# Kernel optimization log

Hardware: AMD Instinct MI355X
Metric: run time of the kernel (lower is better)

## Reference

```python
import jax, jax.numpy as jnp
import numpy as np

# dims matching init_kwargs
D_MODEL = 2048
D_STATE = 64
D_CONV = 4
EXPAND = 2
HEADDIM = 128
NGROUPS = 1
CHUNK = 256
D_INNER = EXPAND * D_MODEL          # 4096
NHEADS = D_INNER // HEADDIM          # 32
CONV_DIM = D_INNER + 2 * NGROUPS * D_STATE      # 4224
D_IN_PROJ = 2 * D_INNER + 2 * NGROUPS * D_STATE + NHEADS  # 8352
BATCH = 2
SEQ = 4096  # multiple of CHUNK -> pad_to_block_length is a no-op
LN_EPS = 1e-5


def setup_inputs() -> dict:
    key = jax.random.key(0)
    ks = jax.random.split(key, 8)
    u = jax.random.normal(ks[0], (BATCH, SEQ, D_MODEL), jnp.float32)
    in_proj_w = jax.random.normal(ks[1], (D_IN_PROJ, D_MODEL), jnp.float32) * 0.02
    in_proj_b = jnp.zeros((D_IN_PROJ,), jnp.float32)
    conv_w = jax.random.normal(ks[2], (CONV_DIM, 1, D_CONV), jnp.float32) * 0.2
    conv_b = jnp.zeros((CONV_DIM,), jnp.float32)
    # dt_bias init as in the module (inverse-softplus of dt in [dt_min, dt_max])
    dt = jnp.exp(jax.random.uniform(ks[3], (NHEADS,), jnp.float32)
                 * (np.log(0.1) - np.log(0.001)) + np.log(0.001))
    dt_bias = dt + jnp.log(-jnp.expm1(-dt))
    A_log = jnp.log(jax.random.uniform(ks[4], (NHEADS,), jnp.float32, 1.0, 16.0))
    ln_w = jnp.ones((D_INNER,), jnp.float32)
    ln_b = jnp.zeros((D_INNER,), jnp.float32)
    out_proj_w = jax.random.normal(ks[5], (D_MODEL, D_INNER), jnp.float32) * 0.02
    out_proj_b = jnp.zeros((D_MODEL,), jnp.float32)
    return dict(u=u, in_proj_w=in_proj_w, in_proj_b=in_proj_b, conv_w=conv_w,
                conv_b=conv_b, dt_bias=dt_bias, A_log=A_log, ln_w=ln_w,
                ln_b=ln_b, out_proj_w=out_proj_w, out_proj_b=out_proj_b)


def segsum(x):
    """x: (..., T) -> (..., T, T) with segsum[i,j] = sum_{j<k<=i} x[k], -inf above diag."""
    T = x.shape[-1]
    lo = jnp.tril(jnp.ones((T, T), bool), -1)
    seg = jnp.cumsum(jnp.where(lo, x[..., :, None], 0.0), axis=-2)
    return jnp.where(jnp.tril(jnp.ones((T, T), bool), 0), seg, -jnp.inf)


def ssd_chunked(X, A, B, C):
    """X:(b,l,h,p) A:(b,l,h) B:(b,l,n) C:(b,l,n) (ngroups=1), chunked SSD scan."""
    b, l, h, p = X.shape
    c = l // CHUNK
    Xc = X.reshape(b, c, CHUNK, h, p)
    Ac = A.reshape(b, c, CHUNK, h).transpose(0, 3, 1, 2)  # b h c l
    Bc = B.reshape(b, c, CHUNK, -1)
    Cc = C.reshape(b, c, CHUNK, -1)
    A_cumsum = jnp.cumsum(Ac, axis=-1)                    # b h c l
    L = jnp.exp(segsum(Ac))                               # b h c l l
    Y_diag = jnp.einsum('bcln,bcsn,bhcls,bcshp->bclhp', Cc, Bc, L, Xc)
    decay_states = jnp.exp(A_cumsum[..., -1:] - A_cumsum)  # b h c l
    states = jnp.einsum('bcln,bhcl,bclhp->bchpn', Bc, decay_states, Xc)
    states = jnp.concatenate([jnp.zeros_like(states[:, :1]), states], axis=1)  # b (c+1) h p n
    A_last = jnp.pad(A_cumsum[..., -1], ((0, 0), (0, 0), (1, 0)))  # b h (c+1)
    decay_chunk = jnp.exp(segsum(A_last))                 # b h (c+1) (c+1)
    new_states = jnp.einsum('bhzc,bchpn->bzhpn', decay_chunk, states)
    inter_states = new_states[:, :-1]                     # b c h p n
    state_decay_out = jnp.exp(A_cumsum)                   # b h c l
    Y_off = jnp.einsum('bcln,bchpn,bhcl->bclhp', Cc, inter_states, state_decay_out)
    return (Y_diag + Y_off).reshape(b, l, h, p)


def reference(u, in_proj_w, in_proj_b, conv_w, conv_b, dt_bias, A_log,
              ln_w, ln_b, out_proj_w, out_proj_b):
    # seqlen already a multiple of CHUNK, so padding is a no-op
    zxbcdt = jnp.einsum('bld,ed->ble', u, in_proj_w) + in_proj_b
    A = -jnp.exp(A_log)                                   # (h,)
    z = zxbcdt[..., :D_INNER]
    xBC = zxbcdt[..., D_INNER:D_INNER + CONV_DIM]
    dt = jax.nn.softplus(zxbcdt[..., D_INNER + CONV_DIM:] + dt_bias)  # (b,l,h)
    # causal depthwise conv1d (pad left d_conv-1, crop to seqlen)
    x_ncl = jnp.transpose(xBC, (0, 2, 1))
    y_ncl = jax.lax.conv_general_dilated(
        x_ncl, conv_w, window_strides=(1,), padding=[(D_CONV - 1, 0)],
        feature_group_count=CONV_DIM, dimension_numbers=('NCH', 'OIH', 'NCH'))
    xBC = jax.nn.silu(jnp.transpose(y_ncl + conv_b[None, :, None], (0, 2, 1)))
    x = xBC[..., :D_INNER].reshape(*xBC.shape[:2], NHEADS, HEADDIM)  # b l h p
    Bm = xBC[..., D_INNER:D_INNER + NGROUPS * D_STATE]                # b l n
    Cm = xBC[..., D_INNER + NGROUPS * D_STATE:]                       # b l n
    y = ssd_chunked(x * dt[..., None], A * dt, Bm, Cm)
    y = y.reshape(*y.shape[:2], D_INNER)
    y = y * jax.nn.silu(z)
    mu = jnp.mean(y, axis=-1, keepdims=True)
    var = jnp.mean(jnp.square(y - mu), axis=-1, keepdims=True)
    y = (y - mu) * jax.lax.rsqrt(var + LN_EPS) * ln_w + ln_b
    out = jnp.einsum('bld,ed->ble', y, out_proj_w) + out_proj_b
    return out
```

## Files before the change

kernel.cpp:

```cpp
#include <hip/hip_runtime.h>
#include <math.h>

#define BATCH    2
#define SEQ      4096
#define DMODEL   2048
#define DSTATE   64
#define HEADDIM  128
#define NHEADS   32
#define DINNER   4096
#define CONVDIM  4224
#define DINPROJ  8352
#define NCHUNK   16
#define CHUNKL   256
#define ROWS     (BATCH*SEQ)

typedef __attribute__((ext_vector_type(8))) __bf16 bf16x8;
typedef __attribute__((ext_vector_type(4))) float floatx4;
typedef __attribute__((ext_vector_type(8))) unsigned short ushort8;
typedef __attribute__((ext_vector_type(2))) unsigned int uint2v;

__device__ __forceinline__ unsigned short f2bf(float f) {
    union { float f; unsigned int u; } v; v.f = f;
    unsigned int u = v.u;
    unsigned int r = (u + 0x7FFFu + ((u >> 16) & 1u)) >> 16;
    return (unsigned short)r;
}
__device__ __forceinline__ float bf2f(unsigned short s) {
    union { unsigned int u; float f; } v; v.u = ((unsigned int)s) << 16;
    return v.f;
}

__device__ __forceinline__ void gload_lds16(const unsigned short* g, unsigned short* lds) {
    __builtin_amdgcn_global_load_lds(
        (const __attribute__((address_space(1))) unsigned int*)g,
        (__attribute__((address_space(3))) unsigned int*)lds,
        16, 0, 0);
}

__device__ __forceinline__ uint2v tr16(const unsigned short* p) {
    uint2v d;
    asm volatile("ds_read_b64_tr_b16 %0, %1"
                 : "=v"(d)
                 : "v"((const __attribute__((address_space(3))) unsigned short*)p));
    return d;
}
union U8tr { uint2v v2[2]; bf16x8 f; };

__device__ __forceinline__ void cvt8(const float* s, unsigned short* d, int i) {
    float4 a = *reinterpret_cast<const float4*>(s + i);
    float4 b = *reinterpret_cast<const float4*>(s + i + 4);
    ushort8 o;
    o[0] = f2bf(a.x); o[1] = f2bf(a.y); o[2] = f2bf(a.z); o[3] = f2bf(a.w);
    o[4] = f2bf(b.x); o[5] = f2bf(b.y); o[6] = f2bf(b.z); o[7] = f2bf(b.w);
    *reinterpret_cast<ushort8*>(d + i) = o;
}

__global__ __launch_bounds__(256) void f32_to_bf16_2(
    const float* __restrict__ s0, unsigned short* __restrict__ d0, int nb0,
    const float* __restrict__ s1, unsigned short* __restrict__ d1)
{
    int b = blockIdx.x;
    if (b < nb0) {
        cvt8(s0, d0, (b * 256 + threadIdx.x) * 8);
    } else {
        cvt8(s1, d1, ((b - nb0) * 256 + threadIdx.x) * 8);
    }
}


#define STAGE(G, ldg, grow0, clampmax, k0, off)                                 \
  { int r0_ = (grow0) + sr0; int r1_ = (grow0) + sr1;                           \
    if ((clampmax) >= 0) { if (r0_ > (clampmax)) r0_ = (clampmax);              \
                           if (r1_ > (clampmax)) r1_ = (clampmax); }            \
    unsigned short* d_ = smem + (off) + ldsw;                                   \
    gload_lds16((G) + (size_t)r0_ * (ldg) + (k0) + sc0, d_);                    \
    gload_lds16((G) + (size_t)r1_ * (ldg) + (k0) + sc1, d_ + 4096); }

__device__ __forceinline__ void rd_a(bf16x8 (&dst)[4][2], const unsigned short* base) {
    #pragma unroll
    for (int mt = 0; mt < 4; ++mt)
        #pragma unroll
        for (int ks = 0; ks < 2; ++ks)
            dst[mt][ks] = *reinterpret_cast<const bf16x8*>(base + (mt * 2 + ks) * 512);
}
__device__ __forceinline__ void rd_b(bf16x8 (&dst)[2][2], const unsigned short* base) {
    #pragma unroll
    for (int nt = 0; nt < 2; ++nt)
        #pragma unroll
        for (int ks = 0; ks < 2; ++ks)
            dst[nt][ks] = *reinterpret_cast<const bf16x8*>(base + (nt * 2 + ks) * 512);
}

template<int R0, int C0>
__device__ __forceinline__ void mfma_q(floatx4 (&acc)[8][4],
                                       const bf16x8 (&a)[4][2],
                                       const bf16x8 (&b)[2][2])
{
    #pragma unroll
    for (int mt = 0; mt < 4; ++mt)
        #pragma unroll
        for (int nt = 0; nt < 2; ++nt) {
            acc[R0+mt][C0+nt] = __builtin_amdgcn_mfma_f32_16x16x32_bf16(a[mt][0], b[nt][0], acc[R0+mt][C0+nt], 0, 0, 0);
            acc[R0+mt][C0+nt] = __builtin_amdgcn_mfma_f32_16x16x32_bf16(a[mt][1], b[nt][1], acc[R0+mt][C0+nt], 0, 0, 0);
        }
}

#define MQ(R0, C0, A_, B_)                          \
    __builtin_amdgcn_s_setprio(1);                  \
    if (alive) mfma_q<R0, C0>(acc, A_, B_);         \
    __builtin_amdgcn_s_setprio(0);

template<int OUT_BF16>
__global__ __launch_bounds__(512, 2) void gemm256(
    const unsigned short* __restrict__ A, int lda,
    const unsigned short* __restrict__ Bt, int ldb,
    const float* __restrict__ bias,
    void* __restrict__ Cp, int ldc,
    int M, int N, int K)
{
    extern __shared__ __align__(16) unsigned short smem[];
    const int tid  = threadIdx.x;
    const int wave = tid >> 6;
    const int lane = tid & 63;
    const int q    = lane >> 4;
    const int lm   = lane & 15;
    const int wm   = wave >> 2;
    const int wn   = wave & 3;
    const int bh   = wn >> 1;
    const int bn2  = wn & 1;

    const int cpx = gridDim.x >> 3;
    const int sid = (blockIdx.x & 7) * cpx + (blockIdx.x >> 3);
    const int nbm = M >> 8;
    const int nbn = gridDim.x / nbm;
    int bm, bn;
    {
        const int GM = 8;
        int nig = GM * nbn;
        int grp = sid / nig;
        int first = grp * GM;
        int gsz = nbm - first; if (gsz > GM) gsz = GM;
        bm = first + (sid % nig) % gsz;
        bn = (sid % nig) / gsz;
    }
    const int arow0 = bm * 256;
    const int brow0 = bn * 256;
    const bool alive = (brow0 + wn * 64) < N;

    int sr0, sc0, sr1, sc1;
    {
        int L = tid << 4;
        int b = L & 1023; b ^= ((b >> 9) & 1) << 5;
        int sub = L >> 10;
        sr0 = ((sub >> 1) << 4) | (b >> 6);
        sc0 = ((sub & 1) << 5) | ((b & 63) >> 1);
        L = 8192 | (tid << 4);
        b = L & 1023; b ^= ((b >> 9) & 1) << 5;
        sub = L >> 10;
        sr1 = ((sub >> 1) << 4) | (b >> 6);
        sc1 = ((sub & 1) << 5) | ((b & 63) >> 1);
    }
    const int ldsw = wave * 512;
    const int lhw = ((((lm << 6) | (q << 4)) ^ ((lm & 8) << 2)) >> 1);
    const int NT  = K >> 6;
    const int NM1 = N - 1;

    STAGE(A,  lda, arow0,       -1,  0,  0);
    STAGE(A,  lda, arow0 + 128, -1,  0,  8192);
    STAGE(Bt, ldb, brow0,       NM1, 0,  16384);
    STAGE(Bt, ldb, brow0 + 128, NM1, 0,  24576);
    STAGE(Bt, ldb, brow0,       NM1, 64, 32768 + 16384);
    STAGE(Bt, ldb, brow0 + 128, NM1, 64, 32768 + 24576);
    STAGE(A,  lda, arow0,       -1,  64, 32768);
    STAGE(A,  lda, arow0 + 128, -1,  64, 32768 + 8192);
    asm volatile("s_waitcnt vmcnt(8)" ::: "memory");
    __builtin_amdgcn_s_barrier();

    const unsigned short* Ab0 = smem + wm * 8192 + lhw;
    const unsigned short* Bb0 = smem + 16384 + bh * 8192 + bn2 * 4096 + lhw;
    const unsigned short* Ab1 = Ab0 + 32768;
    const unsigned short* Bb1 = Bb0 + 32768;

    bf16x8 a_lo[4][2], a_hi[4][2], b_lo[2][2], b_hi[2][2];
    rd_a(a_lo, Ab0);
    rd_b(b_lo, Bb0);

    floatx4 acc[8][4] = {};
    const int NI = NT >> 1;

    for (int i = 0; i < NI; ++i) {
        int tE2 = 2 * i + 2; if (tE2 > NT - 1) tE2 = NT - 1;
        int tO2 = 2 * i + 3; if (tO2 > NT - 1) tO2 = NT - 1;
        const int kE = tE2 << 6, kO = tO2 << 6;

        rd_b(b_hi, Bb0 + 2048);
        __builtin_amdgcn_s_barrier();
        MQ(0, 0, a_lo, b_lo);
        __builtin_amdgcn_s_barrier();

        rd_a(a_hi, Ab0 + 4096);
        STAGE(Bt, ldb, brow0, NM1, kE, 16384);
        __builtin_amdgcn_s_barrier();
        MQ(0, 2, a_lo, b_hi);
        __builtin_amdgcn_s_barrier();

        STAGE(Bt, ldb, brow0 + 128, NM1, kE, 24576);
        STAGE(A,  lda, arow0,       -1,  kE, 0);
        __builtin_amdgcn_s_barrier();
        MQ(4, 2, a_hi, b_hi);
        asm volatile("s_waitcnt vmcnt(6)" ::: "memory");
        __builtin_amdgcn_s_barrier();

        rd_a(a_lo, Ab1);
        rd_b(b_hi, Bb1);
        STAGE(A, lda, arow0 + 128, -1, kE, 8192);
        __builtin_amdgcn_s_barrier();
        MQ(4, 0, a_hi, b_lo);
        __builtin_amdgcn_s_barrier();

        rd_b(b_lo, Bb1 + 2048);
        __builtin_amdgcn_s_barrier();
        MQ(0, 0, a_lo, b_hi);
        __builtin_amdgcn_s_barrier();

        rd_a(a_hi, Ab1 + 4096);
        STAGE(Bt, ldb, brow0, NM1, kO, 32768 + 16384);
        __builtin_amdgcn_s_barrier();
        MQ(0, 2, a_lo, b_lo);
        __builtin_amdgcn_s_barrier();

        STAGE(Bt, ldb, brow0 + 128, NM1, kO, 32768 + 24576);
        STAGE(A,  lda, arow0,       -1,  kO, 32768);
        __builtin_amdgcn_s_barrier();
        MQ(4, 2, a_hi, b_lo);
        asm volatile("s_waitcnt vmcnt(6)" ::: "memory");
        __builtin_amdgcn_s_barrier();

        rd_a(a_lo, Ab0);
        rd_b(b_lo, Bb0);
        STAGE(A, lda, arow0 + 128, -1, kO, 32768 + 8192);
        __builtin_amdgcn_s_barrier();
        MQ(4, 0, a_hi, b_hi);
        __builtin_amdgcn_s_barrier();
    }

    asm volatile("s_waitcnt vmcnt(0)" ::: "memory");

    const int row0 = arow0 + wm * 128;
    const int col0 = brow0 + wn * 64;
    #pragma unroll
    for (int mt = 0; mt < 8; ++mt)
        #pragma unroll
        for (int nt = 0; nt < 4; ++nt) {
            int col = col0 + nt * 16 + lm;
            if (col < N) {
                float bv = bias[col];
                #pragma unroll
                for (int r = 0; r < 4; ++r) {
                    int row = row0 + mt * 16 + q * 4 + r;
                    float v = acc[mt][nt][r] + bv;
                    if (OUT_BF16)
                        ((unsigned short*)Cp)[(size_t)row * ldc + col] = f2bf(v);
                    else
                        ((float*)Cp)[(size_t)row * ldc + col] = v;
                }
            }
        }
}

#define NCONVB (ROWS * (CONVDIM / 8) / 256)

__global__ __launch_bounds__(256) void convdt(
    const unsigned short* __restrict__ zx, const float* __restrict__ conv_w,
    const float* __restrict__ conv_b, unsigned short* __restrict__ xBC,
    const float* __restrict__ dt_bias, const float* __restrict__ A_log,
    float* __restrict__ dtb, float* __restrict__ cum, float* __restrict__ csum)
{
    __shared__ float ws4[4];
    if (blockIdx.x < NCONVB) {
        int idx = blockIdx.x * 256 + threadIdx.x;
        int g   = idx % (CONVDIM / 8);
        int row = idx / (CONVDIM / 8);
        int l   = row & (SEQ - 1);
        int ch0 = g * 8;
        const unsigned short* base = zx + (size_t)row * DINPROJ + DINNER + ch0;
        float s[8];
        float4 w4[8];
        #pragma unroll
        for (int c = 0; c < 8; ++c) {
            s[c]  = conv_b[ch0 + c];
            w4[c] = *reinterpret_cast<const float4*>(conv_w + (ch0 + c) * 4);
        }
        #pragma unroll
        for (int j = 0; j < 4; ++j) {
            int lj = l - 3 + j;
            if (lj >= 0) {
                ushort8 v = *reinterpret_cast<const ushort8*>(base + (long)(lj - l) * DINPROJ);
                #pragma unroll
                for (int c = 0; c < 8; ++c) {
                    float wj = (j == 0) ? w4[c].x : (j == 1) ? w4[c].y : (j == 2) ? w4[c].z : w4[c].w;
                    s[c] += wj * bf2f(v[c]);
                }
            }
        }
        ushort8 o;
        #pragma unroll
        for (int c = 0; c < 8; ++c) {
            float sig = 1.f / (1.f + __expf(-s[c]));
            o[c] = f2bf(s[c] * sig);
        }
        *reinterpret_cast<ushort8*>(xBC + (size_t)row * CONVDIM + ch0) = o;
    } else {
        int id = blockIdx.x - NCONVB;
        int h  = id & 31;
        int c  = (id >> 5) & 15;
        int b  = id >> 9;
        int t  = threadIdx.x;
        int row = b * SEQ + c * CHUNKL + t;
        float v = bf2f(zx[(size_t)row * DINPROJ + DINNER + CONVDIM + h]) + dt_bias[h];
        float dtv = (v > 20.f) ? v : log1pf(__expf(v));
        dtb[row * NHEADS + h] = dtv;
        float adt = -__expf(A_log[h]) * dtv;
        int lane = t & 63, wv = t >> 6;
        float s = adt;
        #pragma unroll
        for (int o = 1; o < 64; o <<= 1) {
            float x = __shfl_up(s, o, 64);
            if (lane >= o) s += x;
        }
        if (lane == 63) ws4[wv] = s;
        __syncthreads();
        float basev = 0.f;
        #pragma unroll
        for (int w = 0; w < 3; ++w)
            if (w < wv) basev += ws4[w];
        s += basev;
        cum[id * 256 + t] = s;
        if (t == 255) csum[id] = s;
    }
}

__global__ __launch_bounds__(256) void score_kernel(
    const unsigned short* __restrict__ xBC, unsigned short* __restrict__ S_raw)
{
    int bc = blockIdx.x;
    int sq = blockIdx.y;
    int tid = threadIdx.x;
    int wave = tid >> 6, lane = tid & 63, q = lane >> 4, lm = lane & 15;
    __shared__ __align__(16) unsigned short Ct[256 * 72];
    __shared__ __align__(16) unsigned short Btl[64 * 72];

    #pragma unroll
    for (int i = 0; i < 8; ++i) {
        int idx = tid + 256 * i;
        int r = idx >> 3, ch = idx & 7;
        ushort8 v = *reinterpret_cast<const ushort8*>(
            &xBC[(size_t)(bc * 256 + r) * CONVDIM + DINNER + DSTATE + ch * 8]);
        *reinterpret_cast<ushort8*>(&Ct[r * 72 + ch * 8]) = v;
    }
    #pragma unroll
    for (int i = 0; i < 2; ++i) {
        int idx = tid + 256 * i;
        int r = idx >> 3, ch = idx & 7;
        ushort8 v = *reinterpret_cast<const ushort8*>(
            &xBC[(size_t)(bc * 256 + sq * 64 + r) * CONVDIM + DINNER + ch * 8]);
        *reinterpret_cast<ushort8*>(&Btl[r * 72 + ch * 8]) = v;
    }
    __syncthreads();

    floatx4 acc[4][4] = {};
    #pragma unroll
    for (int ks = 0; ks < 2; ++ks) {
        bf16x8 af[4], bfv[4];
        #pragma unroll
        for (int mt = 0; mt < 4; ++mt)
            af[mt] = *reinterpret_cast<const bf16x8*>(&Ct[(wave * 64 + mt * 16 + lm) * 72 + ks * 32 + q * 8]);
        #pragma unroll
        for (int nt = 0; nt < 4; ++nt)
            bfv[nt] = *reinterpret_cast<const bf16x8*>(&Btl[(nt * 16 + lm) * 72 + ks * 32 + q * 8]);
        #pragma unroll
        for (int mt = 0; mt < 4; ++mt)
            #pragma unroll
            for (int nt = 0; nt < 4; ++nt)
                acc[mt][nt] = __builtin_amdgcn_mfma_f32_16x16x32_bf16(af[mt], bfv[nt], acc[mt][nt], 0, 0, 0);
    }

    #pragma unroll
    for (int mt = 0; mt < 4; ++mt)
        #pragma unroll
        for (int nt = 0; nt < 4; ++nt) {
            int l = wave * 64 + mt * 16 + q * 4;
            int s = sq * 64 + nt * 16 + lm;
            #pragma unroll
            for (int r = 0; r < 4; ++r)
                S_raw[(size_t)(bc * 256 + l + r) * 256 + s] = f2bf(acc[mt][nt][r]);
        }
}

__global__ __launch_bounds__(256) void states_kernel(
    const unsigned short* __restrict__ xBC, const float* __restrict__ dtb,
    const float* __restrict__ cum, float* __restrict__ states)
{
    int id = blockIdx.x;
    int h  = id & 31;
    int c  = (id >> 5) & 15;
    int b  = id >> 9;
    int tid = threadIdx.x;
    int wave = tid >> 6, lane = tid & 63, q = lane >> 4, lm = lane & 15;

    __shared__ float wls[256];
    __shared__ __align__(16) unsigned short Xs[16 * 8 * 72];
    __shared__ __align__(16) unsigned short Bs[16 * 4 * 72];

    const int cumbase = id * 256;
    const int row0 = b * SEQ + c * CHUNKL;
    {
        float cumlast = cum[cumbase + 255];
        wls[tid] = __expf(cumlast - cum[cumbase + tid]) * dtb[(row0 + tid) * NHEADS + h];
    }

    floatx4 acc[2][4] = {};

    for (int sc = 0; sc < 4; ++sc) {
        const int s0 = sc * 64;
        __syncthreads();
        #pragma unroll
        for (int i = 0; i < 4; ++i) {
            int idx = tid + 256 * i;
            int sr = idx >> 4, ch = idx & 15;
            int row = row0 + s0 + sr;
            ushort8 v = *reinterpret_cast<const ushort8*>(
                &xBC[(size_t)row * CONVDIM + h * HEADDIM + ch * 8]);
            float w = wls[s0 + sr];
            ushort8 o;
            #pragma unroll
            for (int j = 0; j < 8; ++j) o[j] = f2bf(bf2f(v[j]) * w);
            int a = ((sr >> 2) * 8 + (ch >> 1)) * 72 + (sr & 3) * 16 + (ch & 1) * 8;
            *reinterpret_cast<ushort8*>(&Xs[a]) = o;
        }
        #pragma unroll
        for (int i = 0; i < 2; ++i) {
            int idx = tid + 256 * i;
            int sr = idx >> 3, ch = idx & 7;
            int row = row0 + s0 + sr;
            ushort8 v = *reinterpret_cast<const ushort8*>(
                &xBC[(size_t)row * CONVDIM + DINNER + ch * 8]);
            int a = ((sr >> 2) * 4 + (ch >> 1)) * 72 + (sr & 3) * 16 + (ch & 1) * 8;
            *reinterpret_cast<ushort8*>(&Bs[a]) = v;
        }
        __syncthreads();
        #pragma unroll
        for (int ks = 0; ks < 2; ++ks) {
            bf16x8 af[2], bfv[4];
            #pragma unroll
            for (int mt = 0; mt < 2; ++mt) {
                const unsigned short* vp = Xs + ((ks * 8 + 2 * q) * 8 + (wave * 2 + mt)) * 72 + lm * 4;
                U8tr u; u.v2[0] = tr16(vp); u.v2[1] = tr16(vp + 576);
                af[mt] = u.f;
            }
            #pragma unroll
            for (int nt = 0; nt < 4; ++nt) {
                const unsigned short* vp = Bs + ((ks * 8 + 2 * q) * 4 + nt) * 72 + lm * 4;
                U8tr u; u.v2[0] = tr16(vp); u.v2[1] = tr16(vp + 288);
                bfv[nt] = u.f;
            }
            asm volatile("s_waitcnt lgkmcnt(0)" ::: "memory");
            __builtin_amdgcn_sched_barrier(0);
            #pragma unroll
            for (int mt = 0; mt < 2; ++mt)
                #pragma unroll
                for (int nt = 0; nt < 4; ++nt)
                    acc[mt][nt] = __builtin_amdgcn_mfma_f32_16x16x32_bf16(af[mt], bfv[nt], acc[mt][nt], 0, 0, 0);
        }
    }

    #pragma unroll
    for (int mt = 0; mt < 2; ++mt)
        #pragma unroll
        for (int nt = 0; nt < 4; ++nt)
            #pragma unroll
            for (int r = 0; r < 4; ++r) {
                int p = wave * 32 + mt * 16 + q * 4 + r;
                int n = nt * 16 + lm;
                states[(size_t)id * 8192 + p * 64 + n] = acc[mt][nt][r];
            }
}

__global__ __launch_bounds__(256) void inter_kernel(
    float* __restrict__ states, const float* __restrict__ csum)
{
    int idx = blockIdx.x * 256 + threadIdx.x;
    int pn  = idx & 8191;
    int h   = (idx >> 13) & 31;
    int b   = idx >> 18;
    float S = 0.f;
    for (int c = 0; c < 16; ++c) {
        int id = (b * 16 + c) * 32 + h;
        size_t off = (size_t)id * 8192 + pn;
        float st = states[off];
        states[off] = S;
        S = S * __expf(csum[id]) + st;
    }
}

__global__ __launch_bounds__(256) void y_mfma(
    const unsigned short* __restrict__ xBC,
    const unsigned short* __restrict__ S_raw,
    const float* __restrict__ dtb,
    const float* __restrict__ cum,
    const float* __restrict__ inter,
    unsigned short* __restrict__ zx)
{
    int id = blockIdx.x;
    int h  = id & 31;
    int bc = id >> 5;
    const int lh = blockIdx.y;
    int tid = threadIdx.x, wave = tid >> 6, lane = tid & 63, q = lane >> 4, lm = lane & 15;
    int wl = wave >> 1, wp = wave & 1;

    __shared__ float cums[256];
    __shared__ float dts[256];
    __shared__ __align__(16) unsigned short XdtT[128 * 72];
    __shared__ __align__(16) unsigned short PT[128 * 72];

    cums[tid] = cum[id * 256 + tid];
    dts[tid]  = dtb[(size_t)(bc * 256 + tid) * NHEADS + h];
    __syncthreads();

    floatx4 acc[4][4] = {};
    const int l0w = lh * 128 + wl * 64;
    const int nst = 2 * lh + 2;

    for (int st = 0; st < nst; ++st) {
        const int s0 = st * 64;
        __syncthreads();
        #pragma unroll
        for (int i = 0; i < 4; ++i) {
            int idx = tid + 256 * i;
            int sr = idx >> 4, ch = idx & 15;
            int srow = bc * 256 + s0 + sr;
            ushort8 v = *reinterpret_cast<const ushort8*>(
                &xBC[(size_t)srow * CONVDIM + h * HEADDIM + ch * 8]);
            float dt = dts[s0 + sr];
            ushort8 o;
            #pragma unroll
            for (int j = 0; j < 8; ++j) o[j] = f2bf(bf2f(v[j]) * dt);
            int a = ((sr >> 2) * 8 + (ch >> 1)) * 72 + (sr & 3) * 16 + (ch & 1) * 8;
            *reinterpret_cast<ushort8*>(&XdtT[a]) = o;
        }
        const int r0 = (s0 > lh * 128) ? 64 : 0;
        const int iters = (128 - r0) >> 5;
        for (int i = 0; i < iters; ++i) {
            int idx = tid + 256 * i;
            int r = r0 + (idx >> 3), ch = idx & 7;
            int l = lh * 128 + r;
            float cl = cums[l];
            ushort8 v = *reinterpret_cast<const ushort8*>(
                &S_raw[(size_t)(bc * 256 + l) * 256 + s0 + ch * 8]);
            ushort8 o;
            #pragma unroll
            for (int j = 0; j < 8; ++j) {
                int s = s0 + ch * 8 + j;
                float val = (s <= l) ? bf2f(v[j]) * __expf(cl - cums[s]) : 0.f;
                o[j] = f2bf(val);
            }
            *reinterpret_cast<ushort8*>(&PT[r * 72 + ch * 8]) = o;
        }
        __syncthreads();
        if (s0 <= l0w) {
            #pragma unroll
            for (int ks = 0; ks < 2; ++ks) {
                bf16x8 af[4], bfv[4];
                #pragma unroll
                for (int mt = 0; mt < 4; ++mt)
                    af[mt] = *reinterpret_cast<const bf16x8*>(
                        &PT[(wl * 64 + mt * 16 + lm) * 72 + ks * 32 + q * 8]);
                #pragma unroll
                for (int nt = 0; nt < 4; ++nt) {
                    const unsigned short* vp = XdtT + ((ks * 8 + 2 * q) * 8 + (wp * 4 + nt)) * 72 + lm * 4;
                    U8tr u; u.v2[0] = tr16(vp); u.v2[1] = tr16(vp + 576);
                    bfv[nt] = u.f;
                }
                asm volatile("s_waitcnt lgkmcnt(0)" ::: "memory");
                __builtin_amdgcn_sched_barrier(0);
                #pragma unroll
                for (int mt = 0; mt < 4; ++mt)
                    #pragma unroll
                    for (int nt = 0; nt < 4; ++nt)
                        acc[mt][nt] = __builtin_amdgcn_mfma_f32_16x16x32_bf16(af[mt], bfv[nt], acc[mt][nt], 0, 0, 0);
            }
        }
    }

    __syncthreads();
    {
        int p = tid >> 1, n0 = (tid & 1) * 32;
        const float* sp = &inter[(size_t)id * 8192 + p * 64 + n0];
        #pragma unroll
        for (int k2 = 0; k2 < 4; ++k2) {
            float4 a = *reinterpret_cast<const float4*>(sp + k2 * 8);
            float4 b2 = *reinterpret_cast<const float4*>(sp + k2 * 8 + 4);
            ushort8 o;
            o[0] = f2bf(a.x); o[1] = f2bf(a.y); o[2] = f2bf(a.z); o[3] = f2bf(a.w);
            o[4] = f2bf(b2.x); o[5] = f2bf(b2.y); o[6] = f2bf(b2.z); o[7] = f2bf(b2.w);
            *reinterpret_cast<ushort8*>(&XdtT[p * 72 + n0 + k2 * 8]) = o;
        }
        int r = tid >> 1;
        int l = lh * 128 + r;
        float ef = __expf(cums[l]);
        const unsigned short* cp = &xBC[(size_t)(bc * 256 + l) * CONVDIM + DINNER + DSTATE + n0];
        #pragma unroll
        for (int k2 = 0; k2 < 4; ++k2) {
            ushort8 v = *reinterpret_cast<const ushort8*>(cp + k2 * 8);
            ushort8 o;
            #pragma unroll
            for (int j = 0; j < 8; ++j) o[j] = f2bf(bf2f(v[j]) * ef);
            *reinterpret_cast<ushort8*>(&PT[r * 72 + n0 + k2 * 8]) = o;
        }
    }
    __syncthreads();
    #pragma unroll
    for (int ks = 0; ks < 2; ++ks) {
        bf16x8 af[4], bfv[4];
        #pragma unroll
        for (int mt = 0; mt < 4; ++mt)
            af[mt] = *reinterpret_cast<const bf16x8*>(
                &PT[(wl * 64 + mt * 16 + lm) * 72 + ks * 32 + q * 8]);
        #pragma unroll
        for (int nt = 0; nt < 4; ++nt)
            bfv[nt] = *reinterpret_cast<const bf16x8*>(
                &XdtT[(wp * 64 + nt * 16 + lm) * 72 + ks * 32 + q * 8]);
        #pragma unroll
        for (int mt = 0; mt < 4; ++mt)
            #pragma unroll
            for (int nt = 0; nt < 4; ++nt)
                acc[mt][nt] = __builtin_amdgcn_mfma_f32_16x16x32_bf16(af[mt], bfv[nt], acc[mt][nt], 0, 0, 0);
    }

    #pragma unroll
    for (int mt = 0; mt < 4; ++mt)
        #pragma unroll
        for (int nt = 0; nt < 4; ++nt) {
            int l = lh * 128 + wl * 64 + mt * 16 + q * 4;
            int pcol = wp * 64 + nt * 16 + lm;
            #pragma unroll
            for (int r = 0; r < 4; ++r)
                zx[(size_t)(bc * 256 + l + r) * DINPROJ + DINNER + h * HEADDIM + pcol]
                    = f2bf(acc[mt][nt][r]);
        }
}

__global__ __launch_bounds__(256) void gate_ln_cvt(
    unsigned short* __restrict__ zx, const float* __restrict__ ln_w,
    const float* __restrict__ ln_b,
    const float* __restrict__ w2, unsigned short* __restrict__ w2_bf)
{
    __shared__ float rs[256], rq[256];
    if (blockIdx.x >= ROWS) {
        cvt8(w2, w2_bf, ((blockIdx.x - ROWS) * 256 + threadIdx.x) * 8);
        return;
    }
    int row = blockIdx.x;
    int t   = threadIdx.x;
    size_t base = (size_t)row * DINPROJ;
    float g[16];
    float sum = 0.f, sumsq = 0.f;
    #pragma unroll
    for (int j = 0; j < 2; ++j) {
        int i = t * 8 + j * 2048;
        ushort8 zv = *reinterpret_cast<const ushort8*>(zx + base + i);
        ushort8 yv = *reinterpret_cast<const ushort8*>(zx + base + DINNER + i);
        #pragma unroll
        for (int k = 0; k < 8; ++k) {
            float z = bf2f(zv[k]);
            float y = bf2f(yv[k]);
            float sig = 1.f / (1.f + __expf(-z));
            float v = y * z * sig;
            g[j * 8 + k] = v;
            sum += v; sumsq += v * v;
        }
    }
    rs[t] = sum; rq[t] = sumsq;
    __syncthreads();
    for (int off = 128; off > 0; off >>= 1) {
        if (t < off) { rs[t] += rs[t + off]; rq[t] += rq[t + off]; }
        __syncthreads();
    }
    float mu   = rs[0] * (1.f / DINNER);
    float var  = rq[0] * (1.f / DINNER) - mu * mu;
    float rstd = rsqrtf(var + 1e-5f);
    #pragma unroll
    for (int j = 0; j < 2; ++j) {
        int i = t * 8 + j * 2048;
        ushort8 o;
        #pragma unroll
        for (int k = 0; k < 8; ++k)
            o[k] = f2bf((g[j * 8 + k] - mu) * rstd * ln_w[i + k] + ln_b[i + k]);
        *reinterpret_cast<ushort8*>(zx + base + DINNER + i) = o;
    }
}

extern "C" void kernel_launch(void* const* d_in, const int* in_sizes, int n_in,
                              void* d_out, int out_size, void* d_ws, size_t ws_size,
                              hipStream_t stream)
{
    const float* u          = (const float*)d_in[0];
    const float* in_proj_w  = (const float*)d_in[1];
    const float* in_proj_b  = (const float*)d_in[2];
    const float* conv_w     = (const float*)d_in[3];
    const float* conv_b     = (const float*)d_in[4];
    const float* dt_bias    = (const float*)d_in[5];
    const float* A_log      = (const float*)d_in[6];
    const float* ln_w       = (const float*)d_in[7];
    const float* ln_b       = (const float*)d_in[8];
    const float* out_proj_w = (const float*)d_in[9];
    const float* out_proj_b = (const float*)d_in[10];
    float* out = (float*)d_out;

    unsigned short* zx  = (unsigned short*)d_ws;
    unsigned short* xBC = zx + (size_t)ROWS * DINPROJ;
    float* dtb    = (float*)(xBC + (size_t)ROWS * CONVDIM);
    float* cum    = dtb + (size_t)ROWS * NHEADS;
    float* csum   = cum + (size_t)ROWS * NHEADS;
    float* states = csum + 1024;
    unsigned short* S_raw = (unsigned short*)(states + (size_t)1024 * 8192);

    unsigned short* u_bf  = (unsigned short*)states;
    unsigned short* w1_bf = xBC;
    unsigned short* w2_bf = (unsigned short*)states;

    static bool attr_done = false;
    if (!attr_done) {
        hipFuncSetAttribute(reinterpret_cast<const void*>(&gemm256<1>),
                            hipFuncAttributeMaxDynamicSharedMemorySize, 131072);
        hipFuncSetAttribute(reinterpret_cast<const void*>(&gemm256<0>),
                            hipFuncAttributeMaxDynamicSharedMemorySize, 131072);
        attr_done = true;
    }

    dim3 blk(256);

    const int NBU  = (ROWS * DMODEL) / 2048;
    const int NBW1 = (DINPROJ * DMODEL) / 2048;
    f32_to_bf16_2<<<dim3(NBU + NBW1), blk, 0, stream>>>(u, u_bf, NBU, in_proj_w, w1_bf);

    gemm256<1><<<dim3((ROWS / 256) * ((DINPROJ + 255) / 256)), dim3(512), 131072, stream>>>(
        u_bf, DMODEL, w1_bf, DMODEL, in_proj_b, (void*)zx, DINPROJ, ROWS, DINPROJ, DMODEL);

    convdt<<<dim3(NCONVB + BATCH * NCHUNK * NHEADS), blk, 0, stream>>>(
        zx, conv_w, conv_b, xBC, dt_bias, A_log, dtb, cum, csum);

    score_kernel<<<dim3(BATCH * NCHUNK, 4), blk, 0, stream>>>(xBC, S_raw);

    states_kernel<<<dim3(BATCH * NCHUNK * NHEADS), blk, 0, stream>>>(xBC, dtb, cum, states);

    inter_kernel<<<dim3((BATCH * NHEADS * 8192) / 256), blk, 0, stream>>>(states, csum);

    y_mfma<<<dim3(BATCH * NCHUNK * NHEADS, 2), blk, 0, stream>>>(xBC, S_raw, dtb, cum, states, zx);

    gate_ln_cvt<<<dim3(ROWS + (DMODEL * DINNER) / 2048), blk, 0, stream>>>(
        zx, ln_w, ln_b, out_proj_w, w2_bf);

    gemm256<0><<<dim3((ROWS / 256) * (DMODEL / 256)), dim3(512), 131072, stream>>>(
        (const unsigned short*)(zx + DINNER), DINPROJ, w2_bf, DINNER, out_proj_b, (void*)out,
        DMODEL, ROWS, DMODEL, DINNER);
}
```

Before: 889.1 us.

## Drop GEMM pre-MFMA barriers, register-block conv over rows, batch inter-chunk loads

Removes one of the two workgroup barriers around each MFMA quarter in the main GEMM loop, cutting synchronisation stalls. The LDS reads are now ordered only by the remaining barrier, which may be a race risk. The conv kernel now computes four consecutive rows per thread, reusing seven loaded input rows instead of re-reading four per output row. The inter-chunk state scan loads all 16 chunk states up front so the loads overlap rather than serialising with the recurrence.

```diff
diff --git a/kernel.cpp b/kernel.cpp
--- a/kernel.cpp
+++ b/kernel.cpp
@@ -194,19 +194,16 @@
         const int kE = tE2 << 6, kO = tO2 << 6;
 
         rd_b(b_hi, Bb0 + 2048);
-        __builtin_amdgcn_s_barrier();
         MQ(0, 0, a_lo, b_lo);
         __builtin_amdgcn_s_barrier();
 
         rd_a(a_hi, Ab0 + 4096);
         STAGE(Bt, ldb, brow0, NM1, kE, 16384);
-        __builtin_amdgcn_s_barrier();
         MQ(0, 2, a_lo, b_hi);
         __builtin_amdgcn_s_barrier();
 
         STAGE(Bt, ldb, brow0 + 128, NM1, kE, 24576);
         STAGE(A,  lda, arow0,       -1,  kE, 0);
-        __builtin_amdgcn_s_barrier();
         MQ(4, 2, a_hi, b_hi);
         asm volatile("s_waitcnt vmcnt(6)" ::: "memory");
         __builtin_amdgcn_s_barrier();
@@ -214,24 +211,20 @@
         rd_a(a_lo, Ab1);
         rd_b(b_hi, Bb1);
         STAGE(A, lda, arow0 + 128, -1, kE, 8192);
-        __builtin_amdgcn_s_barrier();
         MQ(4, 0, a_hi, b_lo);
         __builtin_amdgcn_s_barrier();
 
         rd_b(b_lo, Bb1 + 2048);
-        __builtin_amdgcn_s_barrier();
         MQ(0, 0, a_lo, b_hi);
         __builtin_amdgcn_s_barrier();
 
         rd_a(a_hi, Ab1 + 4096);
         STAGE(Bt, ldb, brow0, NM1, kO, 32768 + 16384);
-        __builtin_amdgcn_s_barrier();
         MQ(0, 2, a_lo, b_lo);
         __builtin_amdgcn_s_barrier();
 
         STAGE(Bt, ldb, brow0 + 128, NM1, kO, 32768 + 24576);
         STAGE(A,  lda, arow0,       -1,  kO, 32768);
-        __builtin_amdgcn_s_barrier();
         MQ(4, 2, a_hi, b_lo);
         asm volatile("s_waitcnt vmcnt(6)" ::: "memory");
         __builtin_amdgcn_s_barrier();
@@ -239,7 +232,6 @@
         rd_a(a_lo, Ab0);
         rd_b(b_lo, Bb0);
         STAGE(A, lda, arow0 + 128, -1, kO, 32768 + 8192);
-        __builtin_amdgcn_s_barrier();
         MQ(4, 0, a_hi, b_hi);
         __builtin_amdgcn_s_barrier();
     }
@@ -268,7 +260,7 @@
         }
 }
 
-#define NCONVB (ROWS * (CONVDIM / 8) / 256)
+#define NCONVB ((ROWS / 4) * (CONVDIM / 8) / 256)
 
 __global__ __launch_bounds__(256) void convdt(
     const unsigned short* __restrict__ zx, const float* __restrict__ conv_w,
@@ -280,36 +272,43 @@
     if (blockIdx.x < NCONVB) {
         int idx = blockIdx.x * 256 + threadIdx.x;
         int g   = idx % (CONVDIM / 8);
-        int row = idx / (CONVDIM / 8);
-        int l   = row & (SEQ - 1);
+        int rb  = idx / (CONVDIM / 8);
+        int r0  = rb * 4;
+        int l0  = r0 & (SEQ - 1);
         int ch0 = g * 8;
-        const unsigned short* base = zx + (size_t)row * DINPROJ + DINNER + ch0;
-        float s[8];
+        const unsigned short* base = zx + (size_t)r0 * DINPROJ + DINNER + ch0;
         float4 w4[8];
+        float bsv[8];
         #pragma unroll
         for (int c = 0; c < 8; ++c) {
-            s[c]  = conv_b[ch0 + c];
-            w4[c] = *reinterpret_cast<const float4*>(conv_w + (ch0 + c) * 4);
-        }
-        #pragma unroll
-        for (int j = 0; j < 4; ++j) {
-            int lj = l - 3 + j;
+            w4[c]  = *reinterpret_cast<const float4*>(conv_w + (ch0 + c) * 4);
+            bsv[c] = conv_b[ch0 + c];
+        }
+        float vv[7][8];
+        #pragma unroll
+        for (int j = 0; j < 7; ++j) {
+            int lj = l0 - 3 + j;
             if (lj >= 0) {
-                ushort8 v = *reinterpret_cast<const ushort8*>(base + (long)(lj - l) * DINPROJ);
+                ushort8 v = *reinterpret_cast<const ushort8*>(base + (long)(j - 3) * DINPROJ);
                 #pragma unroll
-                for (int c = 0; c < 8; ++c) {
-                    float wj = (j == 0) ? w4[c].x : (j == 1) ? w4[c].y : (j == 2) ? w4[c].z : w4[c].w;
-                    s[c] += wj * bf2f(v[c]);
-                }
+                for (int c = 0; c < 8; ++c) vv[j][c] = bf2f(v[c]);
+            } else {
+                #pragma unroll
+                for (int c = 0; c < 8; ++c) vv[j][c] = 0.f;
             }
         }
-        ushort8 o;
-        #pragma unroll
-        for (int c = 0; c < 8; ++c) {
-            float sig = 1.f / (1.f + __expf(-s[c]));
-            o[c] = f2bf(s[c] * sig);
-        }
-        *reinterpret_cast<ushort8*>(xBC + (size_t)row * CONVDIM + ch0) = o;
+        #pragma unroll
+        for (int i = 0; i < 4; ++i) {
+            ushort8 o;
+            #pragma unroll
+            for (int c = 0; c < 8; ++c) {
+                float s = bsv[c] + w4[c].x * vv[i][c] + w4[c].y * vv[i + 1][c]
+                                 + w4[c].z * vv[i + 2][c] + w4[c].w * vv[i + 3][c];
+                float sig = 1.f / (1.f + __expf(-s));
+                o[c] = f2bf(s * sig);
+            }
+            *reinterpret_cast<ushort8*>(xBC + (size_t)(r0 + i) * CONVDIM + ch0) = o;
+        }
     } else {
         int id = blockIdx.x - NCONVB;
         int h  = id & 31;
@@ -493,13 +492,16 @@
     int pn  = idx & 8191;
     int h   = (idx >> 13) & 31;
     int b   = idx >> 18;
+    float st[16];
+    #pragma unroll
+    for (int c = 0; c < 16; ++c)
+        st[c] = states[(size_t)((b * 16 + c) * 32 + h) * 8192 + pn];
     float S = 0.f;
+    #pragma unroll
     for (int c = 0; c < 16; ++c) {
         int id = (b * 16 + c) * 32 + h;
-        size_t off = (size_t)id * 8192 + pn;
-        float st = states[off];
-        states[off] = S;
-        S = S * __expf(csum[id]) + st;
+        states[(size_t)id * 8192 + pn] = S;
+        S = S * __expf(csum[id]) + st[c];
     }
 }
 
```

New measurement: 768.4 us. -13.6%, faster.
